# Optimization experiments

Hardware: AMD Instinct MI355X
Metric: run time of the kernel (lower is better)

Reference implementation:

```python
import jax, jax.numpy as jnp
import numpy as np

B, NG, H, G, T0, T1 = 4096, 3000, 6, 30, 500, 50  # batch, genes, hidden, genes/term, leaf terms, mid terms
EPS = 1e-5  # BatchNorm1d default eps


def _bn(x, gamma, beta):
    # training-mode BatchNorm1d: biased batch stats over the batch axis
    m = x.mean(axis=0)
    v = ((x - m) ** 2).mean(axis=0)
    return gamma * (x - m) / jnp.sqrt(v + EPS) + beta


def setup_inputs() -> dict:
    key = jax.random.key(0)
    ks = iter(jax.random.split(key, 32))
    rn = lambda shape, s=0.05: jax.random.normal(next(ks), shape, dtype=jnp.float32) * s
    return dict(
        cell_features=jax.random.normal(next(ks), (B, NG), dtype=jnp.float32),
        Wdg=rn((T0 + T1 + 1, G, NG)), bdg=rn((T0 + T1 + 1, G)),
        W0=rn((T0, H, G)), b0=rn((T0, H)), gam0=jnp.ones((T0, H), jnp.float32), bet0=jnp.zeros((T0, H), jnp.float32),
        aw0=rn((T0, H)), ab0=rn((T0,)), av0=rn((T0,)), ac0=rn((T0,)),
        W1=rn((T1, H, 10 * H + G)), b1=rn((T1, H)), gam1=jnp.ones((T1, H), jnp.float32), bet1=jnp.zeros((T1, H), jnp.float32),
        aw1=rn((T1, H)), ab1=rn((T1,)), av1=rn((T1,)), ac1=rn((T1,)),
        W2=rn((H, T1 * H + G)), b2=rn((H,)), gam2=jnp.ones((H,), jnp.float32), bet2=jnp.zeros((H,), jnp.float32),
        aw2=rn((H,)), ab2=rn(()), av2=rn(()), ac2=rn(()),
    )


def reference(cell_features, Wdg, bdg,
              W0, b0, gam0, bet0, aw0, ab0, av0, ac0,
              W1, b1, gam1, bet1, aw1, ab1, av1, ac1,
              W2, b2, gam2, bet2, aw2, ab2, av2, ac2):
    # direct_gene_layer for every term: Linear(ngene -> genes_per_term), no activation
    dg = jnp.einsum('bn,tgn->btg', cell_features, Wdg) + bdg  # [B, 551, G]
    # ---- layer 0 (leaves): input = direct gene output only ----
    z0 = jnp.tanh(jnp.einsum('btg,thg->bth', dg[:, :T0], W0) + b0)
    n0 = _bn(z0, gam0, bet0)                                   # [B, T0, H]
    aux0 = jnp.tanh(jnp.einsum('bth,th->bt', n0, aw0) + ab0) * av0 + ac0
    # ---- layer 1: term t's children are leaves [10t, 10t+10); concat children + direct genes ----
    in1 = jnp.concatenate([n0.reshape(B, T1, 10 * H), dg[:, T0:T0 + T1]], axis=-1)  # [B, T1, 90]
    z1 = jnp.tanh(jnp.einsum('bti,thi->bth', in1, W1) + b1)
    n1 = _bn(z1, gam1, bet1)                                   # [B, T1, H]
    aux1 = jnp.tanh(jnp.einsum('bth,th->bt', n1, aw1) + ab1) * av1 + ac1
    # ---- root: children = all mid terms + direct genes ----
    in2 = jnp.concatenate([n1.reshape(B, T1 * H), dg[:, -1]], axis=-1)  # [B, 330]
    z2 = jnp.tanh(in2 @ W2.T + b2)
    n2 = _bn(z2, gam2, bet2)                                   # [B, H]
    aux2 = jnp.tanh(n2 @ aw2 + ab2) * av2 + ac2                # [B]
    # flatten (aux_out_map, term_NN_out_map) into one array for a single comparable output
    aux_all = jnp.concatenate([aux0, aux1, aux2[:, None]], axis=1)              # [B, 551]
    nn_all = jnp.concatenate([n0.reshape(B, -1), n1.reshape(B, -1), n2], axis=1)  # [B, 551*H]
    return jnp.concatenate([aux_all, nn_all], axis=1)          # [B, 3857]
```

## Files before the change

kernel.cpp:

```cpp
#include <hip/hip_runtime.h>
#include <hip/hip_bf16.h>

#define BATCH 4096
#define NGENE 3000
#define HID   6
#define GPT   30
#define T0N   500
#define T1N   50
#define KP    3008
#define MROWS 4608
#define OUTW  3857
#define BNEPS 1e-5f
#define NIT   94
#define BUFU  12288

typedef __attribute__((ext_vector_type(8))) __bf16 bf16x8;
typedef __attribute__((ext_vector_type(4))) float f32x4;
typedef __attribute__((ext_vector_type(8))) unsigned short ushort8;

__device__ __forceinline__ unsigned short f2bf(float f) {
  unsigned int u = __builtin_bit_cast(unsigned int, f);
  u = (u + 0x7fffu + ((u >> 16) & 1u)) >> 16;
  return (unsigned short)u;
}

__device__ __forceinline__ void gload_lds16(const void* g, void* l) {
  __builtin_amdgcn_global_load_lds(
      (const __attribute__((address_space(1))) unsigned int*)g,
      (__attribute__((address_space(3))) unsigned int*)l, 16, 0, 0);
}

__global__ void prep(const float* __restrict__ cell, const float* __restrict__ Wdg,
                     const float* __restrict__ bdg, const float* __restrict__ W0,
                     const float* __restrict__ b0,
                     ushort8* __restrict__ cellb, ushort8* __restrict__ abuf8,
                     float* __restrict__ bias) {
  int blk = blockIdx.x;
  if (blk < 6016) {
    int idx = blk * 256 + threadIdx.x;
    int r = idx / 376, c8 = idx - r * 376;
    int c = c8 * 8;
    ushort8 o = (ushort8)0;
    if (c < NGENE) {
      const float4* p = (const float4*)(cell + (size_t)r * NGENE + c);
      float4 a = p[0], b = p[1];
      o[0] = f2bf(a.x); o[1] = f2bf(a.y); o[2] = f2bf(a.z); o[3] = f2bf(a.w);
      o[4] = f2bf(b.x); o[5] = f2bf(b.y); o[6] = f2bf(b.z); o[7] = f2bf(b.w);
    }
    cellb[idx] = o;
  } else if (blk < 8378) {
    int idx = (blk - 6016) * 256 + threadIdx.x;
    if (idx >= 1608 * 376) return;
    int r = idx / 376, c8 = idx - r * 376;
    int c = c8 * 8;
    ushort8 o = (ushort8)0;
    if (r < 1530 && c < NGENE) {
      const float4* p = (const float4*)(Wdg + (size_t)(15000 + r) * NGENE + c);
      float4 a = p[0], b = p[1];
      o[0] = f2bf(a.x); o[1] = f2bf(a.y); o[2] = f2bf(a.z); o[3] = f2bf(a.w);
      o[4] = f2bf(b.x); o[5] = f2bf(b.y); o[6] = f2bf(b.z); o[7] = f2bf(b.w);
    }
    abuf8[(size_t)(3000 + r) * 376 + c8] = o;
  } else {
    int idx = (blk - 8378) * 256 + threadIdx.x;
    if (idx >= MROWS) return;
    float v = 0.f;
    if (idx < 3000) {
      int t = idx / HID;
      float s = b0[idx];
#pragma unroll
      for (int g = 0; g < GPT; ++g) s += W0[idx * GPT + g] * bdg[t * GPT + g];
      v = s;
    } else if (idx < 4530) {
      v = bdg[15000 + idx - 3000];
    }
    bias[idx] = v;
  }
}

__global__ void v0_build(const float* __restrict__ Wdg, const float* __restrict__ W0,
                         unsigned short* __restrict__ abuf) {
  int n = blockIdx.x * 256 + threadIdx.x;
  int t = blockIdx.y;
  if (n >= KP) return;
  bool valid = n < NGENE;
  float x[GPT];
#pragma unroll
  for (int g = 0; g < GPT; ++g)
    x[g] = valid ? Wdg[((size_t)(t * GPT + g)) * NGENE + n] : 0.f;
#pragma unroll
  for (int h = 0; h < HID; ++h) {
    const float* w = W0 + (t * HID + h) * GPT;
    float s = 0.f;
#pragma unroll
    for (int g = 0; g < GPT; ++g) s += x[g] * w[g];
    abuf[((size_t)(t * HID + h)) * KP + n] = valid ? f2bf(s) : (unsigned short)0;
  }
}

__global__ __launch_bounds__(512, 2) void gemm_fused(
    const unsigned short* __restrict__ A,
    const unsigned short* __restrict__ Bt,
    const float* __restrict__ bias,
    float* __restrict__ C,
    float* __restrict__ st) {
  extern __shared__ unsigned short smem[];
  const int tid  = threadIdx.x;
  const int wave = tid >> 6, lane = tid & 63;
  const int wm = wave >> 1, wn = wave & 1;
  const int quad = lane >> 4, fr = lane & 15;

  const int bid = blockIdx.x;
  const int wg  = (bid & 7) * 72 + (bid >> 3);
  const int m0 = (wg >> 5) * 256;
  const int n0 = (wg & 31) * 128;

  const int r   = tid >> 2;
  const int ssw = (tid & 3) ^ ((r >> 2) & 3);
  const unsigned short* gA0 = A  + (size_t)(m0 + r) * KP + ssw * 8;
  const unsigned short* gA1 = A  + (size_t)(m0 + 128 + r) * KP + ssw * 8;
  const unsigned short* gB0 = Bt + (size_t)(n0 + r) * KP + ssw * 8;
  const int dA0 = wave * 512;
  const int dA1 = 4096 + wave * 512;
  const int dB0 = 8192 + wave * 512;

  f32x4 acc[4][4] = {};

#pragma unroll
  for (int t = 0; t < 2; ++t) {
    unsigned short* base = smem + t * BUFU;
    gload_lds16(gA0 + t * 32, base + dA0);
    gload_lds16(gA1 + t * 32, base + dA1);
    gload_lds16(gB0 + t * 32, base + dB0);
  }
  asm volatile("s_waitcnt vmcnt(3)" ::: "memory");
  __builtin_amdgcn_s_barrier();

  const int swz  = (quad ^ ((fr >> 2) & 3)) << 3;
  const int aoff = (wm * 64 + fr) * 32 + swz;
  const int boff = 8192 + (wn * 64 + fr) * 32 + swz;

  int cur = 0;
  for (int t = 0; t < NIT; ++t) {
    if (t < NIT - 2) {
      unsigned short* sb = smem + ((cur >= 1) ? cur - 1 : 2) * BUFU;
      const int ko = (t + 2) * 32;
      gload_lds16(gA0 + ko, sb + dA0);
      gload_lds16(gA1 + ko, sb + dA1);
      gload_lds16(gB0 + ko, sb + dB0);
    }
    const unsigned short* buf = smem + cur * BUFU;
    bf16x8 af[4], bf[4];
#pragma unroll
    for (int i = 0; i < 4; ++i) af[i] = *(const bf16x8*)(buf + aoff + i * 512);
#pragma unroll
    for (int j = 0; j < 4; ++j) bf[j] = *(const bf16x8*)(buf + boff + j * 512);
    __builtin_amdgcn_s_setprio(1);
#pragma unroll
    for (int i = 0; i < 4; ++i)
#pragma unroll
      for (int j = 0; j < 4; ++j)
        acc[i][j] = __builtin_amdgcn_mfma_f32_16x16x32_bf16(af[i], bf[j], acc[i][j], 0, 0, 0);
    __builtin_amdgcn_s_setprio(0);
    asm volatile("s_waitcnt lgkmcnt(0)" ::: "memory");
    if (t < NIT - 2) asm volatile("s_waitcnt vmcnt(3)" ::: "memory");
    else             asm volatile("s_waitcnt vmcnt(0)" ::: "memory");
    __builtin_amdgcn_s_barrier();
    cur = (cur == 2) ? 0 : cur + 1;
  }

  const int mbase = m0 + wm * 64 + quad * 4;
  const int nbase = n0 + wn * 64 + fr;
#pragma unroll
  for (int i = 0; i < 4; ++i) {
#pragma unroll
    for (int rr = 0; rr < 4; ++rr) {
      const int m = mbase + i * 16 + rr;
      const float bia = bias[m];
      const bool act = m < 3000;
      float s = 0.f, q = 0.f;
#pragma unroll
      for (int j = 0; j < 4; ++j) {
        float v = acc[i][j][rr] + bia;
        if (act) v = tanhf(v);
        C[(size_t)m * BATCH + nbase + j * 16] = v;
        s += v; q += v * v;
      }
      if (act) {
#pragma unroll
        for (int off = 1; off < 16; off <<= 1) {
          s += __shfl_xor(s, off);
          q += __shfl_xor(q, off);
        }
        if (fr == 0) {
          atomicAdd(&st[2 * m], s);
          atomicAdd(&st[2 * m + 1], q);
        }
      }
    }
  }
}

__global__ void bnfin(const float* __restrict__ st, const float* __restrict__ gam,
                      const float* __restrict__ bet, float* __restrict__ ss, int ncols) {
  int c = blockIdx.x * 256 + threadIdx.x;
  if (c >= ncols) return;
  float m = st[2 * c] * (1.f / BATCH);
  float v = st[2 * c + 1] * (1.f / BATCH) - m * m;
  float sc = gam[c] * rsqrtf(v + BNEPS);
  ss[2 * c] = sc;
  ss[2 * c + 1] = bet[c] - m * sc;
}

__global__ void norm_emit_aux(const float* __restrict__ zT, const float* __restrict__ ss,
                              const float* __restrict__ aw, const float* __restrict__ ab,
                              const float* __restrict__ av, const float* __restrict__ ac,
                              float* __restrict__ out, int ncols, int outoff,
                              int auxoff, int nterm) {
  __shared__ float tile[66][65];
  int lane = threadIdx.x & 63, w = threadIdx.x >> 6;
  int c0 = blockIdx.x * 66, b0 = blockIdx.y * 64;
  for (int cc = w; cc < 66; cc += 4) {
    int c = c0 + cc;
    float n = 0.f;
    if (c < ncols)
      n = zT[(size_t)c * BATCH + b0 + lane] * ss[2 * c] + ss[2 * c + 1];
    tile[cc][lane] = n;
  }
  __syncthreads();
  for (int cl = lane; cl < 66; cl += 64) {
    int c = c0 + cl;
    if (c < ncols) {
#pragma unroll
      for (int i = 0; i < 16; ++i) {
        int rr = w * 16 + i;
        out[(size_t)(b0 + rr) * OUTW + outoff + c] = tile[cl][rr];
      }
    }
  }
  int t0 = c0 / 6;
  for (int tl = w; tl < 11; tl += 4) {
    int t = t0 + tl;
    if (t < nterm && c0 + tl * 6 < ncols) {
      float s = ab[t];
#pragma unroll
      for (int h = 0; h < HID; ++h) s += tile[tl * 6 + h][lane] * aw[t * HID + h];
      out[(size_t)(b0 + lane) * OUTW + auxoff + t] = tanhf(s) * av[t] + ac[t];
    }
  }
}

__global__ void layer1_zT(const float* __restrict__ C, const float* __restrict__ ss0,
                          const float* __restrict__ W1, const float* __restrict__ b1,
                          float* __restrict__ z1T, float* __restrict__ st) {
  int lane = threadIdx.x & 63, tg = threadIdx.x >> 6;
  int t = blockIdx.x * 4 + tg;
  if (t >= T1N) return;
  int b = blockIdx.y * 64 + lane;
  const float* z0T = C;
  const float* dgm = C + (size_t)3000 * BATCH;
  float x[90];
#pragma unroll
  for (int j = 0; j < 60; ++j) {
    int c = t * 60 + j;
    x[j] = z0T[(size_t)c * BATCH + b] * ss0[2 * c] + ss0[2 * c + 1];
  }
#pragma unroll
  for (int g = 0; g < GPT; ++g)
    x[60 + g] = dgm[(size_t)(t * GPT + g) * BATCH + b];
#pragma unroll
  for (int h = 0; h < HID; ++h) {
    int c = t * HID + h;
    const float* w = W1 + c * 90;
    float s = b1[c];
#pragma unroll
    for (int i = 0; i < 90; ++i) s += x[i] * w[i];
    float z = tanhf(s);
    z1T[(size_t)c * BATCH + b] = z;
    float s1 = z, s2 = z * z;
#pragma unroll
    for (int off = 32; off > 0; off >>= 1) {
      s1 += __shfl_down(s1, off);
      s2 += __shfl_down(s2, off);
    }
    if (lane == 0) {
      atomicAdd(&st[2 * c], s1);
      atomicAdd(&st[2 * c + 1], s2);
    }
  }
}

__global__ void root_zT(const float* __restrict__ C, const float* __restrict__ z1T,
                        const float* __restrict__ ss1, const float* __restrict__ W2,
                        const float* __restrict__ b2, float* __restrict__ z2T,
                        float* __restrict__ st) {
  int b = blockIdx.x * 256 + threadIdx.x;
  int lane = threadIdx.x & 63;
  const float* dgr = C + (size_t)4500 * BATCH;
  float s[HID];
#pragma unroll
  for (int h = 0; h < HID; ++h) s[h] = b2[h];
  for (int c = 0; c < 300; ++c) {
    float n = z1T[(size_t)c * BATCH + b] * ss1[2 * c] + ss1[2 * c + 1];
#pragma unroll
    for (int h = 0; h < HID; ++h) s[h] += n * W2[h * 330 + c];
  }
#pragma unroll
  for (int g = 0; g < GPT; ++g) {
    float d = dgr[(size_t)g * BATCH + b];
#pragma unroll
    for (int h = 0; h < HID; ++h) s[h] += d * W2[h * 330 + 300 + g];
  }
#pragma unroll
  for (int h = 0; h < HID; ++h) {
    float z = tanhf(s[h]);
    z2T[(size_t)h * BATCH + b] = z;
    float s1 = z, s2 = z * z;
#pragma unroll
    for (int off = 32; off > 0; off >>= 1) {
      s1 += __shfl_down(s1, off);
      s2 += __shfl_down(s2, off);
    }
    if (lane == 0) {
      atomicAdd(&st[2 * h], s1);
      atomicAdd(&st[2 * h + 1], s2);
    }
  }
}

__global__ void root_emit(const float* __restrict__ z2T, const float* __restrict__ ss2,
                          const float* __restrict__ aw2, const float* __restrict__ ab2,
                          const float* __restrict__ av2, const float* __restrict__ ac2,
                          float* __restrict__ out) {
  int b = blockIdx.x * 256 + threadIdx.x;
  float s = ab2[0];
#pragma unroll
  for (int h = 0; h < HID; ++h) {
    float n = z2T[(size_t)h * BATCH + b] * ss2[2 * h] + ss2[2 * h + 1];
    out[(size_t)b * OUTW + 3851 + h] = n;
    s += n * aw2[h];
  }
  out[(size_t)b * OUTW + 550] = tanhf(s) * av2[0] + ac2[0];
}

extern "C" void kernel_launch(void* const* d_in, const int* in_sizes, int n_in,
                              void* d_out, int out_size, void* d_ws, size_t ws_size,
                              hipStream_t stream) {
  (void)in_sizes; (void)n_in; (void)out_size; (void)ws_size;
  const float* cell = (const float*)d_in[0];
  const float* Wdg  = (const float*)d_in[1];
  const float* bdg  = (const float*)d_in[2];
  const float* W0   = (const float*)d_in[3];
  const float* b0   = (const float*)d_in[4];
  const float* gam0 = (const float*)d_in[5];
  const float* bet0 = (const float*)d_in[6];
  const float* aw0  = (const float*)d_in[7];
  const float* ab0  = (const float*)d_in[8];
  const float* av0  = (const float*)d_in[9];
  const float* ac0  = (const float*)d_in[10];
  const float* W1   = (const float*)d_in[11];
  const float* b1   = (const float*)d_in[12];
  const float* gam1 = (const float*)d_in[13];
  const float* bet1 = (const float*)d_in[14];
  const float* aw1  = (const float*)d_in[15];
  const float* ab1  = (const float*)d_in[16];
  const float* av1  = (const float*)d_in[17];
  const float* ac1  = (const float*)d_in[18];
  const float* W2   = (const float*)d_in[19];
  const float* b2   = (const float*)d_in[20];
  const float* gam2 = (const float*)d_in[21];
  const float* bet2 = (const float*)d_in[22];
  const float* aw2  = (const float*)d_in[23];
  const float* ab2  = (const float*)d_in[24];
  const float* av2  = (const float*)d_in[25];
  const float* ac2  = (const float*)d_in[26];
  float* out = (float*)d_out;

  char* ws = (char*)d_ws;
  unsigned short* cellb = (unsigned short*)(ws);
  unsigned short* abuf  = (unsigned short*)(ws + 24641536);
  float*          C     = (float*)(ws + 52363264);
  float*          z1T   = (float*)(ws + 127860736);
  float*          z2T   = (float*)(ws + 132775936);
  float*          st    = (float*)(ws + 132874240);
  float*          ssb   = (float*)(ws + 132907008);
  float*          bias  = (float*)(ws + 132939776);
  float* st0 = st,  *st1 = st + 2 * 3000,  *st2 = st + 2 * 3300;
  float* ss0 = ssb, *ss1 = ssb + 2 * 3000, *ss2 = ssb + 2 * 3300;

  static int s_attr = 0;
  if (!s_attr) {
    hipFuncSetAttribute(reinterpret_cast<const void*>(gemm_fused),
                        hipFuncAttributeMaxDynamicSharedMemorySize, 73728);
    s_attr = 1;
  }

  hipMemsetAsync(st, 0, 32768, stream);
  prep<<<8396, 256, 0, stream>>>(cell, Wdg, bdg, W0, b0,
                                 (ushort8*)cellb, (ushort8*)abuf, bias);
  v0_build<<<dim3(12, T0N), 256, 0, stream>>>(Wdg, W0, abuf);

  gemm_fused<<<576, 512, 73728, stream>>>(abuf, cellb, bias, C, st0);

  bnfin<<<12, 256, 0, stream>>>(st0, gam0, bet0, ss0, 3000);
  norm_emit_aux<<<dim3(46, 64), 256, 0, stream>>>(C, ss0, aw0, ab0, av0, ac0,
                                                  out, 3000, 551, 0, 500);

  layer1_zT<<<dim3(13, 64), 256, 0, stream>>>(C, ss0, W1, b1, z1T, st1);
  bnfin<<<2, 256, 0, stream>>>(st1, gam1, bet1, ss1, 300);
  norm_emit_aux<<<dim3(5, 64), 256, 0, stream>>>(z1T, ss1, aw1, ab1, av1, ac1,
                                                 out, 300, 3551, 500, 50);

  root_zT<<<16, 256, 0, stream>>>(C, z1T, ss1, W2, b2, z2T, st2);
  bnfin<<<1, 256, 0, stream>>>(st2, gam2, bet2, ss2, 6);
  root_emit<<<16, 256, 0, stream>>>(z2T, ss2, aw2, ab2, av2, ac2, out);
}
```

Before: 678.5 us.

## Retile fused GEMM to 128x128 blocks with K=64 double-buffered LDS stages

The main bf16 GEMM changes from 512-thread blocks on 256x128 tiles with a K=32 triple buffer to 256-thread blocks on 128x128 tiles with a K=64 double buffer. It uses a new XOR swizzle and moves the barrier so the next stage's loads are issued after fragments are read. The goal is fewer loop iterations and barriers per K step and more MFMA work per LDS round trip, with twice as many blocks. In exchange, A-tile reuse per block drops, global loads per output rise, and there is less prefetch depth to hide memory latency.

```diff
diff --git a/kernel.cpp b/kernel.cpp
--- a/kernel.cpp
+++ b/kernel.cpp
@@ -11,8 +11,8 @@
 #define MROWS 4608
 #define OUTW  3857
 #define BNEPS 1e-5f
-#define NIT   94
-#define BUFU  12288
+#define NKT   47
+#define BUFU  16384
 
 typedef __attribute__((ext_vector_type(8))) __bf16 bf16x8;
 typedef __attribute__((ext_vector_type(4))) float f32x4;
@@ -98,7 +98,7 @@
   }
 }
 
-__global__ __launch_bounds__(512, 2) void gemm_fused(
+__global__ __launch_bounds__(256, 2) void gemm_fused(
     const unsigned short* __restrict__ A,
     const unsigned short* __restrict__ Bt,
     const float* __restrict__ bias,
@@ -111,63 +111,74 @@
   const int quad = lane >> 4, fr = lane & 15;
 
   const int bid = blockIdx.x;
-  const int wg  = (bid & 7) * 72 + (bid >> 3);
-  const int m0 = (wg >> 5) * 256;
+  const int wg  = (bid & 7) * 144 + (bid >> 3);
+  const int m0 = (wg >> 5) * 128;
   const int n0 = (wg & 31) * 128;
 
-  const int r   = tid >> 2;
-  const int ssw = (tid & 3) ^ ((r >> 2) & 3);
-  const unsigned short* gA0 = A  + (size_t)(m0 + r) * KP + ssw * 8;
-  const unsigned short* gA1 = A  + (size_t)(m0 + 128 + r) * KP + ssw * 8;
-  const unsigned short* gB0 = Bt + (size_t)(n0 + r) * KP + ssw * 8;
-  const int dA0 = wave * 512;
-  const int dA1 = 4096 + wave * 512;
-  const int dB0 = 8192 + wave * 512;
+  const unsigned short* srcA[4];
+  const unsigned short* srcB[4];
+#pragma unroll
+  for (int i = 0; i < 4; ++i) {
+    int c = i * 256 + tid;
+    int row = c >> 3, sl = c & 7;
+    srcA[i] = A  + (size_t)(m0 + row) * KP + ((sl ^ (row & 7)) << 3);
+    srcB[i] = Bt + (size_t)(n0 + row) * KP + ((sl ^ (row & 7)) << 3);
+  }
 
   f32x4 acc[4][4] = {};
 
-#pragma unroll
-  for (int t = 0; t < 2; ++t) {
-    unsigned short* base = smem + t * BUFU;
-    gload_lds16(gA0 + t * 32, base + dA0);
-    gload_lds16(gA1 + t * 32, base + dA1);
-    gload_lds16(gB0 + t * 32, base + dB0);
-  }
-  asm volatile("s_waitcnt vmcnt(3)" ::: "memory");
+#define STAGE(kt, buf)                                                        \
+  {                                                                           \
+    unsigned short* bb = smem + (buf) * BUFU;                                 \
+    const int ko = (kt) * 64;                                                 \
+    _Pragma("unroll")                                                         \
+    for (int i = 0; i < 4; ++i) {                                             \
+      gload_lds16(srcA[i] + ko, bb + i * 2048 + wave * 512);                  \
+      gload_lds16(srcB[i] + ko, bb + 8192 + i * 2048 + wave * 512);           \
+    }                                                                         \
+  }
+
+  STAGE(0, 0);
+  STAGE(1, 1);
+  asm volatile("s_waitcnt vmcnt(8)" ::: "memory");
   __builtin_amdgcn_s_barrier();
 
-  const int swz  = (quad ^ ((fr >> 2) & 3)) << 3;
-  const int aoff = (wm * 64 + fr) * 32 + swz;
-  const int boff = 8192 + (wn * 64 + fr) * 32 + swz;
+  const int ks0 = (quad ^ (fr & 7)) << 3;
+  const int arow = (wm * 64 + fr) * 64;
+  const int brow = 8192 + (wn * 64 + fr) * 64;
 
   int cur = 0;
-  for (int t = 0; t < NIT; ++t) {
-    if (t < NIT - 2) {
-      unsigned short* sb = smem + ((cur >= 1) ? cur - 1 : 2) * BUFU;
-      const int ko = (t + 2) * 32;
-      gload_lds16(gA0 + ko, sb + dA0);
-      gload_lds16(gA1 + ko, sb + dA1);
-      gload_lds16(gB0 + ko, sb + dB0);
-    }
-    const unsigned short* buf = smem + cur * BUFU;
-    bf16x8 af[4], bf[4];
-#pragma unroll
-    for (int i = 0; i < 4; ++i) af[i] = *(const bf16x8*)(buf + aoff + i * 512);
-#pragma unroll
-    for (int j = 0; j < 4; ++j) bf[j] = *(const bf16x8*)(buf + boff + j * 512);
+  for (int t = 0; t < NKT; ++t) {
+    const unsigned short* Ab = smem + cur * BUFU;
+    bf16x8 af[4][2], bf[4][2];
+#pragma unroll
+    for (int tm = 0; tm < 4; ++tm) {
+      af[tm][0] = *(const bf16x8*)(Ab + arow + tm * 1024 + ks0);
+      af[tm][1] = *(const bf16x8*)(Ab + arow + tm * 1024 + (ks0 ^ 32));
+    }
+#pragma unroll
+    for (int tn = 0; tn < 4; ++tn) {
+      bf[tn][0] = *(const bf16x8*)(Ab + brow + tn * 1024 + ks0);
+      bf[tn][1] = *(const bf16x8*)(Ab + brow + tn * 1024 + (ks0 ^ 32));
+    }
+    asm volatile("s_waitcnt lgkmcnt(0)" ::: "memory");
+    __builtin_amdgcn_s_barrier();
+    if (t + 2 < NKT) STAGE(t + 2, cur);
     __builtin_amdgcn_s_setprio(1);
 #pragma unroll
-    for (int i = 0; i < 4; ++i)
-#pragma unroll
-      for (int j = 0; j < 4; ++j)
-        acc[i][j] = __builtin_amdgcn_mfma_f32_16x16x32_bf16(af[i], bf[j], acc[i][j], 0, 0, 0);
+    for (int s = 0; s < 2; ++s)
+#pragma unroll
+      for (int i = 0; i < 4; ++i)
+#pragma unroll
+        for (int j = 0; j < 4; ++j)
+          acc[i][j] = __builtin_amdgcn_mfma_f32_16x16x32_bf16(af[i][s], bf[j][s], acc[i][j], 0, 0, 0);
     __builtin_amdgcn_s_setprio(0);
-    asm volatile("s_waitcnt lgkmcnt(0)" ::: "memory");
-    if (t < NIT - 2) asm volatile("s_waitcnt vmcnt(3)" ::: "memory");
-    else             asm volatile("s_waitcnt vmcnt(0)" ::: "memory");
+    if (t + 2 < NKT)      asm volatile("s_waitcnt vmcnt(8)" ::: "memory");
+    else if (t + 1 < NKT) asm volatile("s_waitcnt vmcnt(0)" ::: "memory");
     __builtin_amdgcn_s_barrier();
-    cur = (cur == 2) ? 0 : cur + 1;
-  }
+    cur ^= 1;
+  }
+#undef STAGE
 
   const int mbase = m0 + wm * 64 + quad * 4;
   const int nbase = n0 + wn * 64 + fr;
@@ -391,7 +402,7 @@
   static int s_attr = 0;
   if (!s_attr) {
     hipFuncSetAttribute(reinterpret_cast<const void*>(gemm_fused),
-                        hipFuncAttributeMaxDynamicSharedMemorySize, 73728);
+                        hipFuncAttributeMaxDynamicSharedMemorySize, 65536);
     s_attr = 1;
   }
 
@@ -400,7 +411,7 @@
                                  (ushort8*)cellb, (ushort8*)abuf, bias);
   v0_build<<<dim3(12, T0N), 256, 0, stream>>>(Wdg, W0, abuf);
 
-  gemm_fused<<<576, 512, 73728, stream>>>(abuf, cellb, bias, C, st0);
+  gemm_fused<<<1152, 256, 65536, stream>>>(abuf, cellb, bias, C, st0);
 
   bnfin<<<12, 256, 0, stream>>>(st0, gam0, bet0, ss0, 3000);
   norm_emit_aux<<<dim3(46, 64), 256, 0, stream>>>(C, ss0, aw0, ab0, av0, ac0,
```

Result: slower. 699.9 us (+3.1%).
